# Optimization experiments

Measured on AMD Instinct MI355X. Metric: run time of the kernel, lower is better.

Reference implementation:

```python
import jax, jax.numpy as jnp
import numpy as np

USER_NUM = 100000
ITEM_NUM = 100000
DIM = 64
BS = 256


def setup_inputs() -> dict:
    key = jax.random.key(0)
    k1, k2, k3, k4, k5 = jax.random.split(key, 5)
    # xavier_normal-ish scale for embeddings/linear
    user_table = jax.random.normal(k1, (USER_NUM, DIM), dtype=jnp.float32) * 0.1
    item_table = jax.random.normal(k2, (ITEM_NUM, DIM), dtype=jnp.float32) * 0.1
    cls_w = jax.random.normal(k3, (5, DIM), dtype=jnp.float32) * (2.0 / (DIM + 5)) ** 0.5
    cls_b = jnp.zeros((5,), dtype=jnp.float32)
    batch_user = jax.random.randint(k4, (BS,), 0, USER_NUM, dtype=jnp.int64)
    values = jnp.array([[1.0, 2.0, 3.0, 4.0, 5.0]], dtype=jnp.float32)
    return {
        "batch_user": batch_user,
        "user_table": user_table,
        "item_table": item_table,
        "cls_w": cls_w,
        "cls_b": cls_b,
        "values": values,
    }


def reference(batch_user, user_table, item_table, cls_w, cls_b, values):
    # forward_full_items: score every (user, item) pair.
    # Torch materializes h_ui = (u repeated) * (items tiled) of shape
    # [bs*item_num, dim]; mathematically logits = einsum over dim, so we
    # fuse the broadcasted product with the tiny Linear to avoid the
    # huge expanded intermediate while computing identical math.
    u = user_table[batch_user]                       # [bs, dim]
    # logits[b,i,c] = sum_d u[b,d] * item[i,d] * W[c,d] + b[c]
    logits = jnp.einsum('bd,id,cd->bic', u, item_table, cls_w) + cls_b  # [bs, item_num, 5]
    prob = jax.nn.softmax(logits, axis=-1)
    return jnp.sum(prob * values[0], axis=-1)        # [bs, item_num]
```

## Files before the change

### kernel.cpp

```cpp
#include <hip/hip_runtime.h>

#define I_TOTAL 100000
#define DIM 64
#define BS 256

typedef __attribute__((ext_vector_type(8))) short bf16x8;
typedef __attribute__((ext_vector_type(4))) float f32x4;

__device__ inline unsigned pk_bf16(float lo, float hi) {
    unsigned r;
    asm("v_cvt_pk_bf16_f32 %0, %1, %2" : "=v"(r) : "v"(lo), "v"(hi));
    return r;
}

__device__ inline bf16x8 pack8(float4 a, float4 b) {
    union { unsigned u[4]; bf16x8 v; } r;
    r.u[0] = pk_bf16(a.x, a.y);
    r.u[1] = pk_bf16(a.z, a.w);
    r.u[2] = pk_bf16(b.x, b.y);
    r.u[3] = pk_bf16(b.z, b.w);
    return r.v;
}

__global__ __launch_bounds__(256) void gemm_softmax_fused(
    const int* __restrict__ bu, const float* __restrict__ ut,
    const float* __restrict__ it, const float* __restrict__ cw,
    const float* __restrict__ clsb, const float* __restrict__ vals,
    float* __restrict__ out)
{
    __shared__ float ldsb[4224];

    const int blk = blockIdx.x;
    const int r8 = blk & 7;
    const int qq = blk >> 3;
    const int g  = qq & 15;
    const int a  = qq >> 4;
    const int y  = a * 8 + r8;
    if (y >= 98) return;

    const int lane = threadIdx.x & 63;
    const int wave = threadIdx.x >> 6;
    const int col  = lane & 15;
    const int quad = lane >> 4;

    const int b_base = g * 16;
    const int i_base = y * 1024 + wave * 256;

    const float s = 1.4426950408889634f;

    const float* up = ut + (size_t)bu[b_base + col] * DIM + quad * 8;
    float4 u0 = *(const float4*)(up);
    float4 u1 = *(const float4*)(up + 4);
    float4 u2 = *(const float4*)(up + 32);
    float4 u3 = *(const float4*)(up + 36);
    u0.x *= s; u0.y *= s; u0.z *= s; u0.w *= s;
    u1.x *= s; u1.y *= s; u1.z *= s; u1.w *= s;
    u2.x *= s; u2.y *= s; u2.z *= s; u2.w *= s;
    u3.x *= s; u3.y *= s; u3.z *= s; u3.w *= s;

    bf16x8 afr[5][2];
    f32x4 cin[5];
    float vv[5];
#pragma unroll
    for (int c = 0; c < 5; ++c) {
        const float* wp = cw + c * DIM + quad * 8;
        float4 w0 = *(const float4*)(wp);
        float4 w1 = *(const float4*)(wp + 4);
        float4 w2 = *(const float4*)(wp + 32);
        float4 w3 = *(const float4*)(wp + 36);
        float4 m0 = make_float4(u0.x*w0.x, u0.y*w0.y, u0.z*w0.z, u0.w*w0.w);
        float4 m1 = make_float4(u1.x*w1.x, u1.y*w1.y, u1.z*w1.z, u1.w*w1.w);
        float4 m2 = make_float4(u2.x*w2.x, u2.y*w2.y, u2.z*w2.z, u2.w*w2.w);
        float4 m3 = make_float4(u3.x*w3.x, u3.y*w3.y, u3.z*w3.z, u3.w*w3.w);
        afr[c][0] = pack8(m0, m1);
        afr[c][1] = pack8(m2, m3);
        float bc = clsb[c] * s;
        cin[c] = (f32x4){bc, bc, bc, bc};
        vv[c] = vals[c];
    }

    if (y < 97) {
        float* wlds = ldsb + wave * 1056 + quad * 264 + col;
        const float* rlds = ldsb + wave * 1056 + quad * 264 + 4 * col;

        float* op[4];
#pragma unroll
        for (int k = 0; k < 4; ++k)
            op[k] = out + (size_t)(b_base + quad * 4 + k) * I_TOTAL + (i_base + 4 * col);

        const float* bp = it + (size_t)(i_base + col) * DIM + quad * 8;

#pragma unroll 1
        for (int t4 = 0; t4 < 4; ++t4) {
#pragma unroll
            for (int ti = 0; ti < 4; ++ti) {
                const float* p = bp + ti * 1024;
                float4 q0 = *(const float4*)(p);
                float4 q1 = *(const float4*)(p + 4);
                float4 q2 = *(const float4*)(p + 32);
                float4 q3 = *(const float4*)(p + 36);
                bf16x8 b0 = pack8(q0, q1);
                bf16x8 b1 = pack8(q2, q3);
                f32x4 acc[5];
#pragma unroll
                for (int c = 0; c < 5; ++c) {
                    acc[c] = __builtin_amdgcn_mfma_f32_16x16x32_bf16(afr[c][0], b0, cin[c], 0, 0, 0);
                    acc[c] = __builtin_amdgcn_mfma_f32_16x16x32_bf16(afr[c][1], b1, acc[c], 0, 0, 0);
                }
#pragma unroll
                for (int rr = 0; rr < 4; ++rr) {
                    float e0 = __builtin_amdgcn_exp2f(acc[0][rr]);
                    float e1 = __builtin_amdgcn_exp2f(acc[1][rr]);
                    float e2 = __builtin_amdgcn_exp2f(acc[2][rr]);
                    float e3 = __builtin_amdgcn_exp2f(acc[3][rr]);
                    float e4 = __builtin_amdgcn_exp2f(acc[4][rr]);
                    float den = ((e0 + e1) + (e2 + e3)) + e4;
                    float num = e0 * vv[0];
                    num = fmaf(e1, vv[1], num);
                    num = fmaf(e2, vv[2], num);
                    num = fmaf(e3, vv[3], num);
                    num = fmaf(e4, vv[4], num);
                    wlds[rr * 64 + ti * 16] = num * __builtin_amdgcn_rcpf(den);
                }
            }
#pragma unroll
            for (int k = 0; k < 4; ++k) {
                f32x4 o4 = *(const f32x4*)(rlds + k * 64);
                *(f32x4*)op[k] = o4;
                op[k] += 64;
            }
            bp += 4 * 1024;
        }
    } else {
#pragma unroll 1
        for (int t = 0; t < 16; ++t) {
            int i  = i_base + t * 16 + col;
            int ic = i < I_TOTAL ? i : I_TOTAL - 1;
            const float* p2 = it + (size_t)ic * DIM + quad * 8;
            float4 q0 = *(const float4*)(p2);
            float4 q1 = *(const float4*)(p2 + 4);
            float4 q2 = *(const float4*)(p2 + 32);
            float4 q3 = *(const float4*)(p2 + 36);
            bf16x8 b0 = pack8(q0, q1);
            bf16x8 b1 = pack8(q2, q3);
            f32x4 acc[5];
#pragma unroll
            for (int c = 0; c < 5; ++c) {
                acc[c] = __builtin_amdgcn_mfma_f32_16x16x32_bf16(afr[c][0], b0, cin[c], 0, 0, 0);
                acc[c] = __builtin_amdgcn_mfma_f32_16x16x32_bf16(afr[c][1], b1, acc[c], 0, 0, 0);
            }
            if (i < I_TOTAL) {
#pragma unroll
                for (int rr = 0; rr < 4; ++rr) {
                    float e0 = __builtin_amdgcn_exp2f(acc[0][rr]);
                    float e1 = __builtin_amdgcn_exp2f(acc[1][rr]);
                    float e2 = __builtin_amdgcn_exp2f(acc[2][rr]);
                    float e3 = __builtin_amdgcn_exp2f(acc[3][rr]);
                    float e4 = __builtin_amdgcn_exp2f(acc[4][rr]);
                    float den = ((e0 + e1) + (e2 + e3)) + e4;
                    float num = e0 * vv[0];
                    num = fmaf(e1, vv[1], num);
                    num = fmaf(e2, vv[2], num);
                    num = fmaf(e3, vv[3], num);
                    num = fmaf(e4, vv[4], num);
                    out[(size_t)(b_base + quad * 4 + rr) * I_TOTAL + i] =
                        num * __builtin_amdgcn_rcpf(den);
                }
            }
        }
    }
}

extern "C" void kernel_launch(void* const* d_in, const int* in_sizes, int n_in,
                              void* d_out, int out_size, void* d_ws, size_t ws_size,
                              hipStream_t stream) {
    const int*   bu   = (const int*)d_in[0];
    const float* ut   = (const float*)d_in[1];
    const float* it   = (const float*)d_in[2];
    const float* cw   = (const float*)d_in[3];
    const float* cb   = (const float*)d_in[4];
    const float* vals = (const float*)d_in[5];
    float* out = (float*)d_out;
    (void)d_ws; (void)ws_size; (void)in_sizes; (void)n_in; (void)out_size;

    gemm_softmax_fused<<<1664, 256, 0, stream>>>(bu, ut, it, cw, cb, vals, out);
}
```

Measured before the change: 208.6 us.

## Pre-convert item table to bf16 in workspace and prefetch next item fragment

Adds a separate kernel that converts the fp32 item table to bf16 in the workspace before the main GEMM-softmax kernel runs. The main kernel then loads ready-made bf16 fragments instead of fp32 values that it must pack itself. This halves the bytes read for the item table, which every batch-group block reads again. It also double-buffers the next fragment load in registers to hide latency. In exchange it costs an extra launch plus a full read and write pass over the table, and it keeps the old kernel as a fallback when the workspace is too small.

```diff
diff --git a/kernel.cpp b/kernel.cpp
--- a/kernel.cpp
+++ b/kernel.cpp
@@ -6,6 +6,11 @@
 
 typedef __attribute__((ext_vector_type(8))) short bf16x8;
 typedef __attribute__((ext_vector_type(4))) float f32x4;
+
+__device__ inline unsigned short f2bf(float x) {
+    union { float f; unsigned u; } v; v.f = x;
+    return (unsigned short)((v.u + 0x8000u) >> 16);
+}
 
 __device__ inline unsigned pk_bf16(float lo, float hi) {
     unsigned r;
@@ -22,11 +27,24 @@
     return r.v;
 }
 
-__global__ __launch_bounds__(256) void gemm_softmax_fused(
+__global__ __launch_bounds__(256) void conv_items(
+    const float* __restrict__ item, unsigned short* __restrict__ itbf)
+{
+    long t = (long)blockIdx.x * 256 + threadIdx.x;
+    const float4* p = (const float4*)(item + t * 8);
+    float4 a = p[0], b = p[1];
+    ushort4 r0, r1;
+    r0.x = f2bf(a.x); r0.y = f2bf(a.y); r0.z = f2bf(a.z); r0.w = f2bf(a.w);
+    r1.x = f2bf(b.x); r1.y = f2bf(b.y); r1.z = f2bf(b.z); r1.w = f2bf(b.w);
+    ushort4* q = (ushort4*)(itbf + t * 8);
+    q[0] = r0; q[1] = r1;
+}
+
+__global__ __launch_bounds__(256) void gemm_softmax(
+    const unsigned short* __restrict__ itbf,
     const int* __restrict__ bu, const float* __restrict__ ut,
-    const float* __restrict__ it, const float* __restrict__ cw,
-    const float* __restrict__ clsb, const float* __restrict__ vals,
-    float* __restrict__ out)
+    const float* __restrict__ cw, const float* __restrict__ clsb,
+    const float* __restrict__ vals, float* __restrict__ out)
 {
     __shared__ float ldsb[4224];
 
@@ -88,6 +106,150 @@
         for (int k = 0; k < 4; ++k)
             op[k] = out + (size_t)(b_base + quad * 4 + k) * I_TOTAL + (i_base + 4 * col);
 
+        const unsigned short* bp = itbf + (size_t)(i_base + col) * DIM + quad * 8;
+
+        bf16x8 nb0 = *(const bf16x8*)(bp);
+        bf16x8 nb1 = *(const bf16x8*)(bp + 32);
+
+#pragma unroll 1
+        for (int t4 = 0; t4 < 4; ++t4) {
+#pragma unroll
+            for (int ti = 0; ti < 4; ++ti) {
+                bf16x8 b0 = nb0, b1 = nb1;
+                const unsigned short* np = bp + (t4 * 4 + ti + 1) * 1024;
+                nb0 = *(const bf16x8*)(np);
+                nb1 = *(const bf16x8*)(np + 32);
+                f32x4 acc[5];
+#pragma unroll
+                for (int c = 0; c < 5; ++c) {
+                    acc[c] = __builtin_amdgcn_mfma_f32_16x16x32_bf16(afr[c][0], b0, cin[c], 0, 0, 0);
+                    acc[c] = __builtin_amdgcn_mfma_f32_16x16x32_bf16(afr[c][1], b1, acc[c], 0, 0, 0);
+                }
+#pragma unroll
+                for (int rr = 0; rr < 4; ++rr) {
+                    float e0 = __builtin_amdgcn_exp2f(acc[0][rr]);
+                    float e1 = __builtin_amdgcn_exp2f(acc[1][rr]);
+                    float e2 = __builtin_amdgcn_exp2f(acc[2][rr]);
+                    float e3 = __builtin_amdgcn_exp2f(acc[3][rr]);
+                    float e4 = __builtin_amdgcn_exp2f(acc[4][rr]);
+                    float den = ((e0 + e1) + (e2 + e3)) + e4;
+                    float num = e0 * vv[0];
+                    num = fmaf(e1, vv[1], num);
+                    num = fmaf(e2, vv[2], num);
+                    num = fmaf(e3, vv[3], num);
+                    num = fmaf(e4, vv[4], num);
+                    wlds[rr * 64 + ti * 16] = num * __builtin_amdgcn_rcpf(den);
+                }
+            }
+#pragma unroll
+            for (int k = 0; k < 4; ++k) {
+                f32x4 o4 = *(const f32x4*)(rlds + k * 64);
+                *(f32x4*)op[k] = o4;
+                op[k] += 64;
+            }
+        }
+    } else {
+#pragma unroll 1
+        for (int t = 0; t < 16; ++t) {
+            int i  = i_base + t * 16 + col;
+            int ic = i < I_TOTAL ? i : I_TOTAL - 1;
+            const unsigned short* p2 = itbf + (size_t)ic * DIM + quad * 8;
+            bf16x8 b0 = *(const bf16x8*)p2;
+            bf16x8 b1 = *(const bf16x8*)(p2 + 32);
+            f32x4 acc[5];
+#pragma unroll
+            for (int c = 0; c < 5; ++c) {
+                acc[c] = __builtin_amdgcn_mfma_f32_16x16x32_bf16(afr[c][0], b0, cin[c], 0, 0, 0);
+                acc[c] = __builtin_amdgcn_mfma_f32_16x16x32_bf16(afr[c][1], b1, acc[c], 0, 0, 0);
+            }
+            if (i < I_TOTAL) {
+#pragma unroll
+                for (int rr = 0; rr < 4; ++rr) {
+                    float e0 = __builtin_amdgcn_exp2f(acc[0][rr]);
+                    float e1 = __builtin_amdgcn_exp2f(acc[1][rr]);
+                    float e2 = __builtin_amdgcn_exp2f(acc[2][rr]);
+                    float e3 = __builtin_amdgcn_exp2f(acc[3][rr]);
+                    float e4 = __builtin_amdgcn_exp2f(acc[4][rr]);
+                    float den = ((e0 + e1) + (e2 + e3)) + e4;
+                    float num = e0 * vv[0];
+                    num = fmaf(e1, vv[1], num);
+                    num = fmaf(e2, vv[2], num);
+                    num = fmaf(e3, vv[3], num);
+                    num = fmaf(e4, vv[4], num);
+                    out[(size_t)(b_base + quad * 4 + rr) * I_TOTAL + i] =
+                        num * __builtin_amdgcn_rcpf(den);
+                }
+            }
+        }
+    }
+}
+
+__global__ __launch_bounds__(256) void gemm_softmax_fb(
+    const int* __restrict__ bu, const float* __restrict__ ut,
+    const float* __restrict__ it, const float* __restrict__ cw,
+    const float* __restrict__ clsb, const float* __restrict__ vals,
+    float* __restrict__ out)
+{
+    __shared__ float ldsb[4224];
+
+    const int blk = blockIdx.x;
+    const int r8 = blk & 7;
+    const int qq = blk >> 3;
+    const int g  = qq & 15;
+    const int a  = qq >> 4;
+    const int y  = a * 8 + r8;
+    if (y >= 98) return;
+
+    const int lane = threadIdx.x & 63;
+    const int wave = threadIdx.x >> 6;
+    const int col  = lane & 15;
+    const int quad = lane >> 4;
+
+    const int b_base = g * 16;
+    const int i_base = y * 1024 + wave * 256;
+
+    const float s = 1.4426950408889634f;
+
+    const float* up = ut + (size_t)bu[b_base + col] * DIM + quad * 8;
+    float4 u0 = *(const float4*)(up);
+    float4 u1 = *(const float4*)(up + 4);
+    float4 u2 = *(const float4*)(up + 32);
+    float4 u3 = *(const float4*)(up + 36);
+    u0.x *= s; u0.y *= s; u0.z *= s; u0.w *= s;
+    u1.x *= s; u1.y *= s; u1.z *= s; u1.w *= s;
+    u2.x *= s; u2.y *= s; u2.z *= s; u2.w *= s;
+    u3.x *= s; u3.y *= s; u3.z *= s; u3.w *= s;
+
+    bf16x8 afr[5][2];
+    f32x4 cin[5];
+    float vv[5];
+#pragma unroll
+    for (int c = 0; c < 5; ++c) {
+        const float* wp = cw + c * DIM + quad * 8;
+        float4 w0 = *(const float4*)(wp);
+        float4 w1 = *(const float4*)(wp + 4);
+        float4 w2 = *(const float4*)(wp + 32);
+        float4 w3 = *(const float4*)(wp + 36);
+        float4 m0 = make_float4(u0.x*w0.x, u0.y*w0.y, u0.z*w0.z, u0.w*w0.w);
+        float4 m1 = make_float4(u1.x*w1.x, u1.y*w1.y, u1.z*w1.z, u1.w*w1.w);
+        float4 m2 = make_float4(u2.x*w2.x, u2.y*w2.y, u2.z*w2.z, u2.w*w2.w);
+        float4 m3 = make_float4(u3.x*w3.x, u3.y*w3.y, u3.z*w3.z, u3.w*w3.w);
+        afr[c][0] = pack8(m0, m1);
+        afr[c][1] = pack8(m2, m3);
+        float bc = clsb[c] * s;
+        cin[c] = (f32x4){bc, bc, bc, bc};
+        vv[c] = vals[c];
+    }
+
+    if (y < 97) {
+        float* wlds = ldsb + wave * 1056 + quad * 264 + col;
+        const float* rlds = ldsb + wave * 1056 + quad * 264 + 4 * col;
+
+        float* op[4];
+#pragma unroll
+        for (int k = 0; k < 4; ++k)
+            op[k] = out + (size_t)(b_base + quad * 4 + k) * I_TOTAL + (i_base + 4 * col);
+
         const float* bp = it + (size_t)(i_base + col) * DIM + quad * 8;
 
 #pragma unroll 1
@@ -181,7 +343,14 @@
     const float* cb   = (const float*)d_in[4];
     const float* vals = (const float*)d_in[5];
     float* out = (float*)d_out;
-    (void)d_ws; (void)ws_size; (void)in_sizes; (void)n_in; (void)out_size;
-
-    gemm_softmax_fused<<<1664, 256, 0, stream>>>(bu, ut, it, cw, cb, vals, out);
-}
+    unsigned short* itbf = (unsigned short*)d_ws;
+
+    const size_t needed = (size_t)I_TOTAL * DIM * 2;
+
+    if (ws_size >= needed) {
+        conv_items<<<3125, 256, 0, stream>>>(it, itbf);
+        gemm_softmax<<<1664, 256, 0, stream>>>(itbf, bu, ut, cw, cb, vals, out);
+    } else {
+        gemm_softmax_fb<<<1664, 256, 0, stream>>>(bu, ut, it, cw, cb, vals, out);
+    }
+}
```

Measured after the change: 176.9 us. -15.2%, faster.
